# Kernel tuning notes

Measured on AMD Instinct MI355X. Metric: run time of the kernel, lower is better.

## Reference

```python
import math
import jax, jax.numpy as jnp
import numpy as np

EMBED = 512
HEADS = 2
HEAD_DIM = EMBED // HEADS


def setup_inputs() -> dict:
    key = jax.random.key(0)
    ks = jax.random.split(key, 10)
    s = 1.0 / math.sqrt(EMBED)
    return {
        "text_embeds": jax.random.normal(ks[0], (64, 32, EMBED), jnp.float32),
        "video_embeds": jax.random.normal(ks[1], (128, 64, EMBED), jnp.float32),
        "Wq": jax.random.normal(ks[2], (EMBED, EMBED), jnp.float32) * s,
        "bq": jnp.zeros((EMBED,), jnp.float32),
        "Wk": jax.random.normal(ks[3], (EMBED, EMBED), jnp.float32) * s,
        "bk": jnp.zeros((EMBED,), jnp.float32),
        "Wv": jax.random.normal(ks[4], (EMBED, EMBED), jnp.float32) * s,
        "bv": jnp.zeros((EMBED,), jnp.float32),
        "Wo": jax.random.normal(ks[5], (EMBED, EMBED), jnp.float32) * s,
        "bo": jnp.zeros((EMBED,), jnp.float32),
    }


def reference(text_embeds, video_embeds, Wq, bq, Wk, bk, Wv, bv, Wo, bo):
    num_texts, num_words, _ = text_embeds.shape
    num_vids, num_frames, _ = video_embeds.shape
    # projections (torch Linear: x @ W.T + b)
    q = (text_embeds @ Wq.T + bq).reshape(num_texts, num_words, HEADS, HEAD_DIM)
    k = (video_embeds @ Wk.T + bk).reshape(num_vids, num_frames, HEADS, HEAD_DIM)
    v = (video_embeds @ Wv.T + bv).reshape(num_vids, num_frames, HEADS, HEAD_DIM)
    # 5D cross attention logits: [vids, texts, heads, frames, words]
    logits = jnp.einsum('avhd,bthd->abhvt', k, q) / math.sqrt(HEAD_DIM)
    weights = jax.nn.softmax(logits, axis=3)  # softmax over frames
    attn = jnp.einsum('avhd,abhvt->abhtd', v, weights)  # [a,b,h,t,d]
    # faithful to torch: reshape (a,b,h,t,d) -> (a,b,t,h*d) in row-major order
    attn = attn.reshape(num_vids, num_texts, num_words, EMBED)
    attn = attn.mean(axis=0)  # [texts, words, embed]
    return attn @ Wo.T + bo
```

## Files before the change

### kernel.cpp

```cpp
#include <hip/hip_runtime.h>
#include <hip/hip_bf16.h>
#include <math.h>

#define EMBED  512
#define HEADS  2
#define HDIM   256
#define NTEXT  64
#define NWORD  32
#define NVID   128
#define NFRM   64

typedef __attribute__((ext_vector_type(8))) short      short8;
typedef __attribute__((ext_vector_type(8))) unsigned short ushort8;
typedef __attribute__((ext_vector_type(4))) float      float4v;
typedef __attribute__((ext_vector_type(4))) unsigned short ushort4v;

__device__ __forceinline__ unsigned short f2bf(float x) {
    __hip_bfloat16 h = __float2bfloat16(x);
    return *(unsigned short*)&h;
}
__device__ __forceinline__ float bf2f(unsigned short u) {
    __hip_bfloat16 h = *(__hip_bfloat16*)&u;
    return __bfloat162float(h);
}

__global__ __launch_bounds__(256)
void proj_qkv(const float* __restrict__ text, const float* __restrict__ video,
              const float* __restrict__ Wq, const float* __restrict__ bq,
              const float* __restrict__ Wk, const float* __restrict__ bk,
              const float* __restrict__ Wv, const float* __restrict__ bv,
              unsigned short* __restrict__ qout,
              unsigned short* __restrict__ Kgf, unsigned short* __restrict__ Vgf) {
    const int mb = blockIdx.x, nb = blockIdx.y;
    const int bj = nb * 64;
    const float *A, *W, *bias;
    int op, arow, a = 0;
    if (mb < 32)       { op = 0; A = text;  W = Wq; bias = bq; arow = mb * 64; }
    else if (mb < 160) { op = 1; A = video; W = Wk; bias = bk; a = mb - 32;  arow = a * 64; }
    else               { op = 2; A = video; W = Wv; bias = bv; a = mb - 160; arow = a * 64; }

    __shared__ __align__(16) unsigned char smem[64 * 72 * 2 * 2];
    unsigned short (*Ab)[72] = (unsigned short (*)[72])smem;
    unsigned short (*Wb)[72] = (unsigned short (*)[72])(smem + 64 * 72 * 2);
    unsigned short (*Eb)[72] = (unsigned short (*)[72])smem;

    const int tid = threadIdx.x;
    const int w = tid >> 6, lane = tid & 63;
    const int lm = lane & 15, qd = lane >> 4;

    float4v acc[4];
    #pragma unroll
    for (int nt = 0; nt < 4; ++nt) acc[nt] = (float4v){0.f, 0.f, 0.f, 0.f};

    for (int k0 = 0; k0 < 512; k0 += 64) {
        #pragma unroll
        for (int it = 0; it < 4; ++it) {
            const int s = tid + it * 256;
            const int r = s >> 4, c4 = (s & 15) * 4;
            float4v fa = *(const float4v*)&A[(size_t)(arow + r) * 512 + k0 + c4];
            float4v fw = *(const float4v*)&W[(size_t)(bj + r) * 512 + k0 + c4];
            *(ushort4v*)&Ab[r][c4] = (ushort4v){f2bf(fa.x), f2bf(fa.y), f2bf(fa.z), f2bf(fa.w)};
            *(ushort4v*)&Wb[r][c4] = (ushort4v){f2bf(fw.x), f2bf(fw.y), f2bf(fw.z), f2bf(fw.w)};
        }
        __syncthreads();
        #pragma unroll
        for (int kq = 0; kq < 2; ++kq) {
            const short8 af = *(const short8*)&Ab[w * 16 + lm][kq * 32 + qd * 8];
            #pragma unroll
            for (int nt = 0; nt < 4; ++nt) {
                const short8 bf = *(const short8*)&Wb[nt * 16 + lm][kq * 32 + qd * 8];
                acc[nt] = __builtin_amdgcn_mfma_f32_16x16x32_bf16(af, bf, acc[nt], 0, 0, 0);
            }
        }
        __syncthreads();
    }

    if (op == 0) {
        #pragma unroll
        for (int nt = 0; nt < 4; ++nt) {
            const int c = bj + nt * 16 + lm;
            const float bb = bias[c];
            #pragma unroll
            for (int reg = 0; reg < 4; ++reg) {
                const int r = arow + w * 16 + qd * 4 + reg;
                qout[(size_t)r * 512 + c] = f2bf((acc[nt][reg] + bb) * 0.0625f);
            }
        }
        return;
    }

    const int h = bj >> 8;
    const int bj_rel = bj & 255;

    if (op == 1) {
        #pragma unroll
        for (int nt = 0; nt < 4; ++nt) {
            const int dl = nt * 16 + lm;
            const float bb = bias[bj + dl];
            #pragma unroll
            for (int reg = 0; reg < 4; ++reg)
                Eb[w * 16 + qd * 4 + reg][dl] = f2bf(acc[nt][reg] + bb);
        }
        __syncthreads();
        const size_t base = ((size_t)(h * 128 + a)) * 16384;
        #pragma unroll
        for (int i = 0; i < 2; ++i) {
            const int s = tid + i * 256;
            const int ntf = s >> 7, kqr = (s >> 6) & 1, l = s & 63;
            const int v = ntf * 16 + (l & 15);
            const int dl = kqr * 32 + (l >> 4) * 8;
            ushort8 val = *(const ushort8*)&Eb[v][dl];
            *(ushort8*)&Kgf[base + ((size_t)(ntf * 8 + (bj_rel >> 5) + kqr) * 64 + l) * 8] = val;
        }
    } else {
        #pragma unroll
        for (int nt = 0; nt < 4; ++nt) {
            const int dl = nt * 16 + lm;
            const float bb = bias[bj + dl];
            #pragma unroll
            for (int reg = 0; reg < 4; ++reg)
                Eb[dl][w * 16 + qd * 4 + reg] = f2bf(acc[nt][reg] + bb);
        }
        __syncthreads();
        const size_t base = ((size_t)(h * 128 + a)) * 16384;
        #pragma unroll
        for (int i = 0; i < 2; ++i) {
            const int s = tid + i * 256;
            const int ntr = s >> 7, kqv = (s >> 6) & 1, l = s & 63;
            const int dl = ntr * 16 + (l & 15);
            const int v0 = kqv * 32 + (l >> 4) * 8;
            ushort8 val = *(const ushort8*)&Eb[dl][v0];
            *(ushort8*)&Vgf[base + ((size_t)(((bj_rel >> 4) + ntr) * 2 + kqv) * 64 + l) * 8] = val;
        }
    }
}

__global__ __launch_bounds__(512, 2)
void attn8(const unsigned short* __restrict__ Kgf,
           const unsigned short* __restrict__ Vgf,
           const unsigned short* __restrict__ q,
           unsigned short* __restrict__ partg) {
    const int c  = blockIdx.x;
    const int h  = blockIdx.y;
    const int tg = blockIdx.z;
    const int tid = threadIdx.x;
    const int w = tid >> 6, lane = tid & 63;
    const int lm = lane & 15, qd = lane >> 4;
    const int wt = w >> 1, wm = w & 1;
    const int b = tg * 4 + wt;

    __shared__ __align__(16) unsigned short KfL[16384];
    __shared__ __align__(16) unsigned short VfL[16384];
    __shared__ __align__(16) unsigned short PfL[8192];
    const int wpf = w * 1024;

    short8 qf[8];
    #pragma unroll
    for (int kq = 0; kq < 8; ++kq)
        qf[kq] = *(const short8*)
            &q[((size_t)(b * 32 + wm * 16 + lm)) * 512 + h * 256 + kq * 32 + qd * 8];

    float4v pacc[16];
    #pragma unroll
    for (int nt = 0; nt < 16; ++nt) pacc[nt] = (float4v){0.f, 0.f, 0.f, 0.f};

    ushort8 rK[4], rV[4];
    {
        const size_t kb = ((size_t)(h * 128 + c * 16)) * 16384;
        #pragma unroll
        for (int i = 0; i < 4; ++i) {
            const int s = tid + i * 512;
            rK[i] = *(const ushort8*)&Kgf[kb + (size_t)s * 8];
            rV[i] = *(const ushort8*)&Vgf[kb + (size_t)s * 8];
        }
    }

    for (int ai = 0; ai < 16; ++ai) {
        __syncthreads();
        #pragma unroll
        for (int i = 0; i < 4; ++i) {
            const int s = tid + i * 512;
            *(ushort8*)&KfL[s * 8] = rK[i];
            *(ushort8*)&VfL[s * 8] = rV[i];
        }
        __syncthreads();
        if (ai < 15) {
            const size_t kb = ((size_t)(h * 128 + c * 16 + ai + 1)) * 16384;
            #pragma unroll
            for (int i = 0; i < 4; ++i) {
                const int s = tid + i * 512;
                rK[i] = *(const ushort8*)&Kgf[kb + (size_t)s * 8];
                rV[i] = *(const ushort8*)&Vgf[kb + (size_t)s * 8];
            }
        }

        float4v lacc[4];
        #pragma unroll
        for (int nt = 0; nt < 4; ++nt) lacc[nt] = (float4v){0.f, 0.f, 0.f, 0.f};
        #pragma unroll
        for (int kq = 0; kq < 8; ++kq) {
            #pragma unroll
            for (int nt = 0; nt < 4; ++nt) {
                const short8 kf = *(const short8*)&KfL[((nt * 8 + kq) * 64 + lane) * 8];
                lacc[nt] = __builtin_amdgcn_mfma_f32_16x16x32_bf16(qf[kq], kf, lacc[nt], 0, 0, 0);
            }
        }
        #pragma unroll
        for (int reg = 0; reg < 4; ++reg) {
            const float l0 = lacc[0][reg], l1 = lacc[1][reg];
            const float l2 = lacc[2][reg], l3 = lacc[3][reg];
            float m = fmaxf(fmaxf(l0, l1), fmaxf(l2, l3));
            m = fmaxf(m, __shfl_xor(m, 1));
            m = fmaxf(m, __shfl_xor(m, 2));
            m = fmaxf(m, __shfl_xor(m, 4));
            m = fmaxf(m, __shfl_xor(m, 8));
            const float e0 = __expf(l0 - m), e1 = __expf(l1 - m);
            const float e2 = __expf(l2 - m), e3 = __expf(l3 - m);
            float s = e0 + e1 + e2 + e3;
            s += __shfl_xor(s, 1);
            s += __shfl_xor(s, 2);
            s += __shfl_xor(s, 4);
            s += __shfl_xor(s, 8);
            const float inv = 1.f / s;
            const int lt = qd * 4 + reg;
            const int jj = lm & 7;
            const int lsub = lt + 16 * (lm >> 3);
            PfL[wpf + (0 * 64 + lsub) * 8 + jj]      = f2bf(e0 * inv);
            PfL[wpf + (0 * 64 + lsub + 32) * 8 + jj] = f2bf(e1 * inv);
            PfL[wpf + (1 * 64 + lsub) * 8 + jj]      = f2bf(e2 * inv);
            PfL[wpf + (1 * 64 + lsub + 32) * 8 + jj] = f2bf(e3 * inv);
        }
        #pragma unroll
        for (int kqv = 0; kqv < 2; ++kqv) {
            const short8 pf = *(const short8*)&PfL[wpf + (kqv * 64 + lane) * 8];
            #pragma unroll
            for (int nt = 0; nt < 16; ++nt) {
                const short8 vf = *(const short8*)&VfL[((nt * 2 + kqv) * 64 + lane) * 8];
                pacc[nt] = __builtin_amdgcn_mfma_f32_16x16x32_bf16(pf, vf, pacc[nt], 0, 0, 0);
            }
        }
    }

    unsigned short* part = partg + (size_t)c * 1048576;
    #pragma unroll
    for (int nt = 0; nt < 16; ++nt) {
        const int d = nt * 16 + lm;
        #pragma unroll
        for (int reg = 0; reg < 4; ++reg) {
            const int t = wm * 16 + qd * 4 + reg;
            const int row = b * 32 + h * 16 + (t >> 1);
            const int col = (t & 1) * 256 + d;
            part[(size_t)row * 512 + col] = f2bf(pacc[nt][reg]);
        }
    }
}

__global__ __launch_bounds__(256)
void reduce8(unsigned short* __restrict__ partg) {
    const size_t i = ((size_t)blockIdx.x * 256 + threadIdx.x) * 8;
    float s[8];
    #pragma unroll
    for (int j = 0; j < 8; ++j) s[j] = 0.f;
    #pragma unroll
    for (int p = 0; p < 8; ++p) {
        ushort8 u = *(const ushort8*)&partg[(size_t)p * 1048576 + i];
        #pragma unroll
        for (int j = 0; j < 8; ++j) s[j] += bf2f(u[j]);
    }
    ushort8 o;
    #pragma unroll
    for (int j = 0; j < 8; ++j) o[j] = f2bf(s[j] * 0.0078125f);
    *(ushort8*)&partg[i] = o;
}

__global__ __launch_bounds__(256)
void proj_o(const unsigned short* __restrict__ Abf, const float* __restrict__ W,
            const float* __restrict__ bias, float* __restrict__ C) {
    __shared__ __align__(16) unsigned short Ab[64][72];
    __shared__ __align__(16) unsigned short Wb[64][72];
    const int tid = threadIdx.x;
    const int bi = blockIdx.x * 64, bj = blockIdx.y * 64;
    const int w = tid >> 6, lane = tid & 63;
    const int lm = lane & 15, qd = lane >> 4;

    float4v acc[4];
    #pragma unroll
    for (int nt = 0; nt < 4; ++nt) acc[nt] = (float4v){0.f, 0.f, 0.f, 0.f};

    for (int k0 = 0; k0 < 512; k0 += 64) {
        #pragma unroll
        for (int it = 0; it < 2; ++it) {
            const int s = tid + it * 256;
            const int r = s >> 3, c8 = (s & 7) * 8;
            *(ushort8*)&Ab[r][c8] = *(const ushort8*)&Abf[(size_t)(bi + r) * 512 + k0 + c8];
        }
        #pragma unroll
        for (int it = 0; it < 4; ++it) {
            const int s = tid + it * 256;
            const int r = s >> 4, c4 = (s & 15) * 4;
            float4v fw = *(const float4v*)&W[(size_t)(bj + r) * 512 + k0 + c4];
            *(ushort4v*)&Wb[r][c4] = (ushort4v){f2bf(fw.x), f2bf(fw.y), f2bf(fw.z), f2bf(fw.w)};
        }
        __syncthreads();
        #pragma unroll
        for (int kq = 0; kq < 2; ++kq) {
            const short8 af = *(const short8*)&Ab[w * 16 + lm][kq * 32 + qd * 8];
            #pragma unroll
            for (int nt = 0; nt < 4; ++nt) {
                const short8 bf = *(const short8*)&Wb[nt * 16 + lm][kq * 32 + qd * 8];
                acc[nt] = __builtin_amdgcn_mfma_f32_16x16x32_bf16(af, bf, acc[nt], 0, 0, 0);
            }
        }
        __syncthreads();
    }
    #pragma unroll
    for (int nt = 0; nt < 4; ++nt) {
        const int cc = bj + nt * 16 + lm;
        const float bb = bias[cc];
        #pragma unroll
        for (int reg = 0; reg < 4; ++reg) {
            const int r = bi + w * 16 + qd * 4 + reg;
            C[(size_t)r * 512 + cc] = acc[nt][reg] + bb;
        }
    }
}

extern "C" void kernel_launch(void* const* d_in, const int* in_sizes, int n_in,
                              void* d_out, int out_size, void* d_ws, size_t ws_size,
                              hipStream_t stream) {
    const float* text  = (const float*)d_in[0];
    const float* video = (const float*)d_in[1];
    const float* Wq = (const float*)d_in[2];
    const float* bq = (const float*)d_in[3];
    const float* Wk = (const float*)d_in[4];
    const float* bk = (const float*)d_in[5];
    const float* Wv = (const float*)d_in[6];
    const float* bv = (const float*)d_in[7];
    const float* Wo = (const float*)d_in[8];
    const float* bo = (const float*)d_in[9];

    unsigned short* Kgf   = (unsigned short*)d_ws;
    unsigned short* Vgf   = (unsigned short*)((char*)d_ws + (8u << 20));
    unsigned short* partg = (unsigned short*)((char*)d_ws + (16u << 20));
    unsigned short* qbf   = (unsigned short*)d_out;
    float*          out   = (float*)d_out;

    proj_qkv<<<dim3(288, 8), 256, 0, stream>>>(text, video, Wq, bq, Wk, bk, Wv, bv,
                                               qbf, Kgf, Vgf);
    attn8<<<dim3(8, 2, 16), 512, 0, stream>>>(Kgf, Vgf, qbf, partg);
    reduce8<<<dim3(512), 256, 0, stream>>>(partg);
    proj_o<<<dim3(32, 8), 256, 0, stream>>>(partg, Wo, bo, out);
}
```

Before: 187.8 us.

## Pre-convert inputs to bf16 and double-buffer attention K/V via direct LDS loads

Adds a separate kernel that converts the text, video and three weight matrices to bf16 once, so the projection GEMM loads bf16 tiles directly instead of converting fp32 on every tile load. The attention kernel is restructured: each warp pair now splits the frames in half, with the softmax combined across the pair through shared memory. K/V are double-buffered in LDS using global_load_lds async copies, replacing the previous register staging. This adds an extra kernel launch and extra barriers per iteration, and uses more LDS, which may cut occupancy.

```diff
diff --git a/kernel.cpp b/kernel.cpp
--- a/kernel.cpp
+++ b/kernel.cpp
@@ -24,20 +24,49 @@
     return __bfloat162float(h);
 }
 
+__device__ __forceinline__ void gload_lds16(unsigned short* dst, const unsigned short* src) {
+#if __has_builtin(__builtin_amdgcn_global_load_lds)
+    __builtin_amdgcn_global_load_lds((const __attribute__((address_space(1))) void*)src,
+                                     (__attribute__((address_space(3))) void*)dst,
+                                     16, 0, 0);
+#else
+    *(ushort8*)dst = *(const ushort8*)src;
+#endif
+}
+
 __global__ __launch_bounds__(256)
-void proj_qkv(const float* __restrict__ text, const float* __restrict__ video,
-              const float* __restrict__ Wq, const float* __restrict__ bq,
-              const float* __restrict__ Wk, const float* __restrict__ bk,
-              const float* __restrict__ Wv, const float* __restrict__ bv,
+void cvt5(const float* __restrict__ s0, const float* __restrict__ s1,
+          const float* __restrict__ s2, const float* __restrict__ s3,
+          const float* __restrict__ s4, unsigned short* __restrict__ dst) {
+    const int y = blockIdx.y;
+    const float* s; size_t off; int n4;
+    if (y == 0)      { s = s0; off = 0;       n4 = 262144;  }
+    else if (y == 1) { s = s1; off = 1048576; n4 = 1048576; }
+    else if (y == 2) { s = s2; off = 5242880; n4 = 65536;   }
+    else if (y == 3) { s = s3; off = 5505024; n4 = 65536;   }
+    else             { s = s4; off = 5767168; n4 = 65536;   }
+    unsigned short* d = dst + off;
+    for (int i = blockIdx.x * 256 + threadIdx.x; i < n4; i += 512 * 256) {
+        float4v f = ((const float4v*)s)[i];
+        ((ushort4v*)d)[i] = (ushort4v){f2bf(f.x), f2bf(f.y), f2bf(f.z), f2bf(f.w)};
+    }
+}
+
+__global__ __launch_bounds__(256)
+void proj_qkv(const unsigned short* __restrict__ text, const unsigned short* __restrict__ video,
+              const unsigned short* __restrict__ Wqb, const float* __restrict__ bq,
+              const unsigned short* __restrict__ Wkb, const float* __restrict__ bk,
+              const unsigned short* __restrict__ Wvb, const float* __restrict__ bv,
               unsigned short* __restrict__ qout,
               unsigned short* __restrict__ Kgf, unsigned short* __restrict__ Vgf) {
     const int mb = blockIdx.x, nb = blockIdx.y;
     const int bj = nb * 64;
-    const float *A, *W, *bias;
+    const unsigned short *A, *W;
+    const float* bias;
     int op, arow, a = 0;
-    if (mb < 32)       { op = 0; A = text;  W = Wq; bias = bq; arow = mb * 64; }
-    else if (mb < 160) { op = 1; A = video; W = Wk; bias = bk; a = mb - 32;  arow = a * 64; }
-    else               { op = 2; A = video; W = Wv; bias = bv; a = mb - 160; arow = a * 64; }
+    if (mb < 32)       { op = 0; A = text;  W = Wqb; bias = bq; arow = mb * 64; }
+    else if (mb < 160) { op = 1; A = video; W = Wkb; bias = bk; a = mb - 32;  arow = a * 64; }
+    else               { op = 2; A = video; W = Wvb; bias = bv; a = mb - 160; arow = a * 64; }
 
     __shared__ __align__(16) unsigned char smem[64 * 72 * 2 * 2];
     unsigned short (*Ab)[72] = (unsigned short (*)[72])smem;
@@ -54,13 +83,11 @@
 
     for (int k0 = 0; k0 < 512; k0 += 64) {
         #pragma unroll
-        for (int it = 0; it < 4; ++it) {
+        for (int it = 0; it < 2; ++it) {
             const int s = tid + it * 256;
-            const int r = s >> 4, c4 = (s & 15) * 4;
-            float4v fa = *(const float4v*)&A[(size_t)(arow + r) * 512 + k0 + c4];
-            float4v fw = *(const float4v*)&W[(size_t)(bj + r) * 512 + k0 + c4];
-            *(ushort4v*)&Ab[r][c4] = (ushort4v){f2bf(fa.x), f2bf(fa.y), f2bf(fa.z), f2bf(fa.w)};
-            *(ushort4v*)&Wb[r][c4] = (ushort4v){f2bf(fw.x), f2bf(fw.y), f2bf(fw.z), f2bf(fw.w)};
+            const int r = s >> 3, c8 = (s & 7) * 8;
+            *(ushort8*)&Ab[r][c8] = *(const ushort8*)&A[(size_t)(arow + r) * 512 + k0 + c8];
+            *(ushort8*)&Wb[r][c8] = *(const ushort8*)&W[(size_t)(bj + r) * 512 + k0 + c8];
         }
         __syncthreads();
         #pragma unroll
@@ -136,7 +163,7 @@
 }
 
 __global__ __launch_bounds__(512, 2)
-void attn8(const unsigned short* __restrict__ Kgf,
+void attn9(const unsigned short* __restrict__ Kgf,
            const unsigned short* __restrict__ Vgf,
            const unsigned short* __restrict__ q,
            unsigned short* __restrict__ partg) {
@@ -146,113 +173,150 @@
     const int tid = threadIdx.x;
     const int w = tid >> 6, lane = tid & 63;
     const int lm = lane & 15, qd = lane >> 4;
-    const int wt = w >> 1, wm = w & 1;
+    const int wt = w >> 1;
+    const int fh = w & 1;
     const int b = tg * 4 + wt;
 
-    __shared__ __align__(16) unsigned short KfL[16384];
-    __shared__ __align__(16) unsigned short VfL[16384];
-    __shared__ __align__(16) unsigned short PfL[8192];
-    const int wpf = w * 1024;
-
-    short8 qf[8];
-    #pragma unroll
-    for (int kq = 0; kq < 8; ++kq)
-        qf[kq] = *(const short8*)
-            &q[((size_t)(b * 32 + wm * 16 + lm)) * 512 + h * 256 + kq * 32 + qd * 8];
-
-    float4v pacc[16];
-    #pragma unroll
-    for (int nt = 0; nt < 16; ++nt) pacc[nt] = (float4v){0.f, 0.f, 0.f, 0.f};
-
-    ushort8 rK[4], rV[4];
-    {
-        const size_t kb = ((size_t)(h * 128 + c * 16)) * 16384;
-        #pragma unroll
-        for (int i = 0; i < 4; ++i) {
-            const int s = tid + i * 512;
-            rK[i] = *(const ushort8*)&Kgf[kb + (size_t)s * 8];
-            rV[i] = *(const ushort8*)&Vgf[kb + (size_t)s * 8];
-        }
-    }
+    __shared__ __align__(16) unsigned short Kb[2][16384];
+    __shared__ __align__(16) unsigned short Vb[2][16384];
+    __shared__ __align__(16) unsigned short Pf[4][2][2][512];
+    __shared__ __align__(16) float Ex[4][2][2][16][2];
+
+    short8 qf[2][8];
+    #pragma unroll
+    for (int mt = 0; mt < 2; ++mt)
+        #pragma unroll
+        for (int kq = 0; kq < 8; ++kq)
+            qf[mt][kq] = *(const short8*)
+                &q[((size_t)(b * 32 + mt * 16 + lm)) * 512 + h * 256 + kq * 32 + qd * 8];
+
+    float4v pacc[2][8];
+    #pragma unroll
+    for (int mt = 0; mt < 2; ++mt)
+        #pragma unroll
+        for (int nd = 0; nd < 8; ++nd) pacc[mt][nd] = (float4v){0.f, 0.f, 0.f, 0.f};
+
+    const size_t vb0 = (size_t)(h * 128 + c * 16) * 16384;
+
+    #pragma unroll
+    for (int i = 0; i < 4; ++i) {
+        const int s = tid + i * 512;
+        gload_lds16(&Kb[0][(size_t)s * 8], &Kgf[vb0 + (size_t)s * 8]);
+        gload_lds16(&Vb[0][(size_t)s * 8], &Vgf[vb0 + (size_t)s * 8]);
+    }
+    #pragma unroll
+    for (int i = 0; i < 4; ++i) {
+        const int s = tid + i * 512;
+        gload_lds16(&Kb[1][(size_t)s * 8], &Kgf[vb0 + 16384 + (size_t)s * 8]);
+        gload_lds16(&Vb[1][(size_t)s * 8], &Vgf[vb0 + 16384 + (size_t)s * 8]);
+    }
+    __syncthreads();
 
     for (int ai = 0; ai < 16; ++ai) {
-        __syncthreads();
-        #pragma unroll
-        for (int i = 0; i < 4; ++i) {
-            const int s = tid + i * 512;
-            *(ushort8*)&KfL[s * 8] = rK[i];
-            *(ushort8*)&VfL[s * 8] = rV[i];
-        }
-        __syncthreads();
-        if (ai < 15) {
-            const size_t kb = ((size_t)(h * 128 + c * 16 + ai + 1)) * 16384;
+        const int cur = ai & 1;
+
+        float4v lacc[2][2];
+        #pragma unroll
+        for (int nt = 0; nt < 2; ++nt)
+            #pragma unroll
+            for (int mt = 0; mt < 2; ++mt) lacc[nt][mt] = (float4v){0.f, 0.f, 0.f, 0.f};
+        #pragma unroll
+        for (int kq = 0; kq < 8; ++kq) {
+            #pragma unroll
+            for (int nt = 0; nt < 2; ++nt) {
+                const short8 kf = *(const short8*)
+                    &Kb[cur][(((fh * 2 + nt) * 8 + kq) * 64 + lane) * 8];
+                lacc[nt][0] = __builtin_amdgcn_mfma_f32_16x16x32_bf16(kf, qf[0][kq], lacc[nt][0], 0, 0, 0);
+                lacc[nt][1] = __builtin_amdgcn_mfma_f32_16x16x32_bf16(kf, qf[1][kq], lacc[nt][1], 0, 0, 0);
+            }
+        }
+
+        float m2[2], sv[2], e[2][2][4];
+        #pragma unroll
+        for (int mt = 0; mt < 2; ++mt) {
+            float mm = lacc[0][mt][0];
+            #pragma unroll
+            for (int nt = 0; nt < 2; ++nt)
+                #pragma unroll
+                for (int r = 0; r < 4; ++r) mm = fmaxf(mm, lacc[nt][mt][r]);
+            mm = fmaxf(mm, __shfl_xor(mm, 16));
+            mm = fmaxf(mm, __shfl_xor(mm, 32));
+            float ss = 0.f;
+            #pragma unroll
+            for (int nt = 0; nt < 2; ++nt)
+                #pragma unroll
+                for (int r = 0; r < 4; ++r) {
+                    const float ev = __expf(lacc[nt][mt][r] - mm);
+                    e[mt][nt][r] = ev;
+                    ss += ev;
+                }
+            ss += __shfl_xor(ss, 16);
+            ss += __shfl_xor(ss, 32);
+            m2[mt] = mm; sv[mt] = ss;
+            if (qd == 0) {
+                Ex[wt][fh][mt][lm][0] = mm;
+                Ex[wt][fh][mt][lm][1] = ss;
+            }
+        }
+        __syncthreads();
+
+        #pragma unroll
+        for (int mt = 0; mt < 2; ++mt) {
+            const float om = Ex[wt][fh ^ 1][mt][lm][0];
+            const float os = Ex[wt][fh ^ 1][mt][lm][1];
+            const float M   = fmaxf(m2[mt], om);
+            const float den = sv[mt] * __expf(m2[mt] - M) + os * __expf(om - M);
+            const float fac = __expf(m2[mt] - M) / den;
+            #pragma unroll
+            for (int nt = 0; nt < 2; ++nt) {
+                ushort4v pv;
+                pv.x = f2bf(e[mt][nt][0] * fac);
+                pv.y = f2bf(e[mt][nt][1] * fac);
+                pv.z = f2bf(e[mt][nt][2] * fac);
+                pv.w = f2bf(e[mt][nt][3] * fac);
+                *(ushort4v*)&Pf[wt][mt][fh][(lm + 16 * (nt * 2 + (qd >> 1))) * 8 + (qd & 1) * 4] = pv;
+            }
+        }
+        __syncthreads();
+
+        #pragma unroll
+        for (int kqv = 0; kqv < 2; ++kqv) {
+            const short8 pf0 = *(const short8*)&Pf[wt][0][kqv][lane * 8];
+            const short8 pf1 = *(const short8*)&Pf[wt][1][kqv][lane * 8];
+            #pragma unroll
+            for (int nd = 0; nd < 8; ++nd) {
+                const short8 vf = *(const short8*)
+                    &Vb[cur][(((fh * 8 + nd) * 2 + kqv) * 64 + lane) * 8];
+                pacc[0][nd] = __builtin_amdgcn_mfma_f32_16x16x32_bf16(pf0, vf, pacc[0][nd], 0, 0, 0);
+                pacc[1][nd] = __builtin_amdgcn_mfma_f32_16x16x32_bf16(pf1, vf, pacc[1][nd], 0, 0, 0);
+            }
+        }
+        __syncthreads();
+
+        if (ai < 14) {
+            const size_t kb = vb0 + (size_t)(ai + 2) * 16384;
             #pragma unroll
             for (int i = 0; i < 4; ++i) {
                 const int s = tid + i * 512;
-                rK[i] = *(const ushort8*)&Kgf[kb + (size_t)s * 8];
-                rV[i] = *(const ushort8*)&Vgf[kb + (size_t)s * 8];
-            }
-        }
-
-        float4v lacc[4];
-        #pragma unroll
-        for (int nt = 0; nt < 4; ++nt) lacc[nt] = (float4v){0.f, 0.f, 0.f, 0.f};
-        #pragma unroll
-        for (int kq = 0; kq < 8; ++kq) {
-            #pragma unroll
-            for (int nt = 0; nt < 4; ++nt) {
-                const short8 kf = *(const short8*)&KfL[((nt * 8 + kq) * 64 + lane) * 8];
-                lacc[nt] = __builtin_amdgcn_mfma_f32_16x16x32_bf16(qf[kq], kf, lacc[nt], 0, 0, 0);
-            }
-        }
-        #pragma unroll
-        for (int reg = 0; reg < 4; ++reg) {
-            const float l0 = lacc[0][reg], l1 = lacc[1][reg];
-            const float l2 = lacc[2][reg], l3 = lacc[3][reg];
-            float m = fmaxf(fmaxf(l0, l1), fmaxf(l2, l3));
-            m = fmaxf(m, __shfl_xor(m, 1));
-            m = fmaxf(m, __shfl_xor(m, 2));
-            m = fmaxf(m, __shfl_xor(m, 4));
-            m = fmaxf(m, __shfl_xor(m, 8));
-            const float e0 = __expf(l0 - m), e1 = __expf(l1 - m);
-            const float e2 = __expf(l2 - m), e3 = __expf(l3 - m);
-            float s = e0 + e1 + e2 + e3;
-            s += __shfl_xor(s, 1);
-            s += __shfl_xor(s, 2);
-            s += __shfl_xor(s, 4);
-            s += __shfl_xor(s, 8);
-            const float inv = 1.f / s;
-            const int lt = qd * 4 + reg;
-            const int jj = lm & 7;
-            const int lsub = lt + 16 * (lm >> 3);
-            PfL[wpf + (0 * 64 + lsub) * 8 + jj]      = f2bf(e0 * inv);
-            PfL[wpf + (0 * 64 + lsub + 32) * 8 + jj] = f2bf(e1 * inv);
-            PfL[wpf + (1 * 64 + lsub) * 8 + jj]      = f2bf(e2 * inv);
-            PfL[wpf + (1 * 64 + lsub + 32) * 8 + jj] = f2bf(e3 * inv);
-        }
-        #pragma unroll
-        for (int kqv = 0; kqv < 2; ++kqv) {
-            const short8 pf = *(const short8*)&PfL[wpf + (kqv * 64 + lane) * 8];
-            #pragma unroll
-            for (int nt = 0; nt < 16; ++nt) {
-                const short8 vf = *(const short8*)&VfL[((nt * 2 + kqv) * 64 + lane) * 8];
-                pacc[nt] = __builtin_amdgcn_mfma_f32_16x16x32_bf16(pf, vf, pacc[nt], 0, 0, 0);
+                gload_lds16(&Kb[cur][(size_t)s * 8], &Kgf[kb + (size_t)s * 8]);
+                gload_lds16(&Vb[cur][(size_t)s * 8], &Vgf[kb + (size_t)s * 8]);
             }
         }
     }
 
     unsigned short* part = partg + (size_t)c * 1048576;
     #pragma unroll
-    for (int nt = 0; nt < 16; ++nt) {
-        const int d = nt * 16 + lm;
-        #pragma unroll
-        for (int reg = 0; reg < 4; ++reg) {
-            const int t = wm * 16 + qd * 4 + reg;
-            const int row = b * 32 + h * 16 + (t >> 1);
-            const int col = (t & 1) * 256 + d;
-            part[(size_t)row * 512 + col] = f2bf(pacc[nt][reg]);
-        }
-    }
+    for (int mt = 0; mt < 2; ++mt)
+        #pragma unroll
+        for (int nd = 0; nd < 8; ++nd)
+            #pragma unroll
+            for (int r = 0; r < 4; ++r) {
+                const int t = mt * 16 + qd * 4 + r;
+                const int d = fh * 128 + nd * 16 + lm;
+                const int row = b * 32 + h * 16 + (t >> 1);
+                const int col = (t & 1) * 256 + d;
+                part[(size_t)row * 512 + col] = f2bf(pacc[mt][nd][r]);
+            }
 }
 
 __global__ __launch_bounds__(256)
@@ -342,12 +406,18 @@
     unsigned short* Kgf   = (unsigned short*)d_ws;
     unsigned short* Vgf   = (unsigned short*)((char*)d_ws + (8u << 20));
     unsigned short* partg = (unsigned short*)((char*)d_ws + (16u << 20));
+    unsigned short* textbf  = partg;
+    unsigned short* videobf = partg + 1048576;
+    unsigned short* wqbf    = partg + 5242880;
+    unsigned short* wkbf    = partg + 5505024;
+    unsigned short* wvbf    = partg + 5767168;
     unsigned short* qbf   = (unsigned short*)d_out;
     float*          out   = (float*)d_out;
 
-    proj_qkv<<<dim3(288, 8), 256, 0, stream>>>(text, video, Wq, bq, Wk, bk, Wv, bv,
-                                               qbf, Kgf, Vgf);
-    attn8<<<dim3(8, 2, 16), 512, 0, stream>>>(Kgf, Vgf, qbf, partg);
+    cvt5<<<dim3(512, 5), 256, 0, stream>>>(text, video, Wq, Wk, Wv, partg);
+    proj_qkv<<<dim3(288, 8), 256, 0, stream>>>(textbf, videobf, wqbf, bq, wkbf, bk,
+                                               wvbf, bv, qbf, Kgf, Vgf);
+    attn9<<<dim3(8, 2, 16), 512, 0, stream>>>(Kgf, Vgf, qbf, partg);
     reduce8<<<dim3(512), 256, 0, stream>>>(partg);
     proj_o<<<dim3(32, 8), 256, 0, stream>>>(partg, Wo, bo, out);
 }
```

Result: faster. 172.5 us (-8.1%).
